# Kernel optimization log

Hardware: AMD Instinct MI355X
Metric: run time of the kernel (lower is better)

Reference implementation:

```python
import jax, jax.numpy as jnp
import numpy as np

B, T, D = 2, 2048, 1024
H = 16
DH = D // H            # 64, per-head dim
C = 128                # d_kv_compress
ROPE_BASE = 10000.0


def _rope_cos_sin(t_len, d_head, dtype):
    # freqs: (T, d_head/2); emb = cat(freqs, freqs) -> (T, d_head)
    inv_freq = 1.0 / (ROPE_BASE ** (jnp.arange(0, d_head, 2, dtype=jnp.float32) / d_head))
    freqs = jnp.arange(t_len, dtype=jnp.float32)[:, None] * inv_freq[None, :]
    emb = jnp.concatenate([freqs, freqs], axis=-1)
    return jnp.cos(emb).astype(dtype), jnp.sin(emb).astype(dtype)


def _rotate_half(x):
    x1, x2 = jnp.split(x, 2, axis=-1)
    return jnp.concatenate([-x2, x1], axis=-1)


def _apply_rope(x, cos, sin):
    # x: (B,H,T,DH); cos/sin: (T,DH)
    return x * cos[None, None] + _rotate_half(x) * sin[None, None]


def setup_inputs() -> dict:
    key = jax.random.key(0)
    ks = jax.random.split(key, 12)
    s = 0.02
    return {
        "x": jax.random.normal(ks[0], (B, T, D), dtype=jnp.float32),
        "w_dk": jax.random.normal(ks[1], (D, C), dtype=jnp.float32) * s,
        "b_dk": jnp.zeros((C,), dtype=jnp.float32),
        "w_dv": jax.random.normal(ks[2], (D, C), dtype=jnp.float32) * s,
        "b_dv": jnp.zeros((C,), dtype=jnp.float32),
        "w_uk": jax.random.normal(ks[3], (C, D), dtype=jnp.float32) * s,
        "b_uk": jnp.zeros((D,), dtype=jnp.float32),
        "w_uv": jax.random.normal(ks[4], (C, D), dtype=jnp.float32) * s,
        "b_uv": jnp.zeros((D,), dtype=jnp.float32),
        "w_o": jax.random.normal(ks[5], (D, D), dtype=jnp.float32) * s,
        "b_o": jnp.zeros((D,), dtype=jnp.float32),
    }


def reference(x, w_dk, b_dk, w_dv, b_dv, w_uk, b_uk, w_uv, b_uv, w_o, b_o):
    Bx, Tx, Dx = x.shape
    # low-rank KV compression then up-projection
    c_k = x @ w_dk + b_dk                      # (B,T,C)
    c_v = x @ w_dv + b_dv                      # (B,T,C)
    k = c_k @ w_uk + b_uk                      # (B,T,D)
    v = c_v @ w_uv + b_uv                      # (B,T,D)

    def split_heads(t):  # (B,T,D) -> (B,H,T,DH)
        return t.reshape(Bx, Tx, H, DH).transpose(0, 2, 1, 3)

    q = split_heads(x)
    k = split_heads(k)
    v = split_heads(v)

    cos, sin = _rope_cos_sin(Tx, DH, x.dtype)
    q = _apply_rope(q, cos, sin)
    k = _apply_rope(k, cos, sin)

    scale = 1.0 / np.sqrt(DH)
    attn = jnp.einsum('bhid,bhjd->bhij', q, k) * scale
    attn = jax.nn.softmax(attn, axis=-1)
    out = jnp.einsum('bhij,bhjd->bhid', attn, v)   # (B,H,T,DH)
    out = out.transpose(0, 2, 1, 3).reshape(Bx, Tx, Dx)
    return out @ w_o + b_o
```

## Files before the change

### kernel.cpp

```cpp
#include <hip/hip_runtime.h>
#include <hip/hip_bf16.h>
#include <math.h>

constexpr int kB  = 2;
constexpr int kT  = 2048;
constexpr int kD  = 1024;
constexpr int kH  = 16;
constexpr int kDH = 64;
constexpr int kC  = 128;
constexpr int kM  = kB * kT;
constexpr int kBH = kB * kH;

#define LOG10000_OVER_32 0.28782313662425575f
#define QSCALE 0.1803368801111773f

typedef unsigned short ushort_t;
using short8 = __attribute__((ext_vector_type(8))) short;
using f32x4  = __attribute__((ext_vector_type(4))) float;

__device__ inline ushort_t f2bf(float f) {
    __hip_bfloat16 h = __float2bfloat16(f);
    return *reinterpret_cast<ushort_t*>(&h);
}

__device__ inline short8 cvt8(const float* p) {
    float4 f0 = *reinterpret_cast<const float4*>(p);
    float4 f1 = *reinterpret_cast<const float4*>(p + 4);
    short8 v;
    v[0] = (short)f2bf(f0.x); v[1] = (short)f2bf(f0.y);
    v[2] = (short)f2bf(f0.z); v[3] = (short)f2bf(f0.w);
    v[4] = (short)f2bf(f1.x); v[5] = (short)f2bf(f1.y);
    v[6] = (short)f2bf(f1.z); v[7] = (short)f2bf(f1.w);
    return v;
}

__global__ __launch_bounds__(256)
void wtrans(const float* __restrict__ w_dk, const float* __restrict__ w_dv,
            const float* __restrict__ w_uk, const float* __restrict__ w_uv,
            const float* __restrict__ w_o,
            ushort_t* __restrict__ dkT, ushort_t* __restrict__ dvT,
            ushort_t* __restrict__ ukT, ushort_t* __restrict__ uvT,
            ushort_t* __restrict__ oT, float2* __restrict__ tab) {
    if (blockIdx.z == 5) {
        int flat = blockIdx.y * 32 + blockIdx.x;
        if (flat >= kT / 8) return;
        int t = flat * 8 + (threadIdx.x >> 5);
        int i = threadIdx.x & 31;
        float inv_freq = expf(-(float)i * LOG10000_OVER_32);
        float s, c;
        sincosf((float)t * inv_freq, &s, &c);
        tab[t * 32 + i] = make_float2(c, s);
        return;
    }
    const float* src; ushort_t* dst; int R, C;
    switch (blockIdx.z) {
        case 0: src = w_dk; dst = dkT; R = kD; C = kC; break;
        case 1: src = w_dv; dst = dvT; R = kD; C = kC; break;
        case 2: src = w_uk; dst = ukT; R = kC; C = kD; break;
        case 3: src = w_uv; dst = uvT; R = kC; C = kD; break;
        default: src = w_o; dst = oT;  R = kD; C = kD; break;
    }
    int c0 = blockIdx.x * 32, r0 = blockIdx.y * 32;
    if (c0 >= C || r0 >= R) return;

    __shared__ float Tl[32][33];
    int tx = threadIdx.x & 31, ty = threadIdx.x >> 5;
#pragma unroll
    for (int i = 0; i < 4; ++i)
        Tl[ty + 8 * i][tx] = src[(size_t)(r0 + ty + 8 * i) * C + c0 + tx];
    __syncthreads();
#pragma unroll
    for (int i = 0; i < 4; ++i)
        dst[(size_t)(c0 + ty + 8 * i) * R + r0 + tx] = f2bf(Tl[tx][ty + 8 * i]);
}

template<int MODE0, int MODE1>
__global__ __launch_bounds__(256)
void gemm_mfma(const ushort_t* __restrict__ A0_, const ushort_t* __restrict__ A1_,
               const ushort_t* __restrict__ Wt0, const float* __restrict__ bias0, void* __restrict__ C0,
               const ushort_t* __restrict__ Wt1, const float* __restrict__ bias1, void* __restrict__ C1,
               const float2* __restrict__ tab, int M, int N, int K) {
    constexpr int LDT = 40;
    __shared__ __align__(16) ushort_t As[128 * LDT];
    __shared__ __align__(16) ushort_t Bs[128 * LDT];

    const ushort_t* A    = blockIdx.z ? A1_ : A0_;
    const ushort_t* Wt   = blockIdx.z ? Wt1 : Wt0;
    const float*    bias = blockIdx.z ? bias1 : bias0;
    void*           Cc   = blockIdx.z ? C1 : C0;
    const int       mode = blockIdx.z ? MODE1 : MODE0;

    const int tid  = threadIdx.x;
    const int wave = tid >> 6, lane = tid & 63;
    const int g = lane >> 4, cl = lane & 15;
    const int m0 = blockIdx.y * 128, n0 = blockIdx.x * 128;
    const int wm = (wave >> 1) * 64, wn = (wave & 1) * 64;

    const int ar = tid >> 1;
    const int ac = (tid & 1) * 16;

    f32x4 acc[4][4] = {};

    for (int k0 = 0; k0 < K; k0 += 32) {
        {
            const ushort_t* Ab = A + (size_t)(m0 + ar) * K + k0 + ac;
            *reinterpret_cast<short8*>(&As[ar * LDT + ac])     = *reinterpret_cast<const short8*>(Ab);
            *reinterpret_cast<short8*>(&As[ar * LDT + ac + 8]) = *reinterpret_cast<const short8*>(Ab + 8);
            const ushort_t* Wb = Wt + (size_t)(n0 + ar) * K + k0 + ac;
            *reinterpret_cast<short8*>(&Bs[ar * LDT + ac])     = *reinterpret_cast<const short8*>(Wb);
            *reinterpret_cast<short8*>(&Bs[ar * LDT + ac + 8]) = *reinterpret_cast<const short8*>(Wb + 8);
        }
        __syncthreads();

        short8 a[4], b[4];
#pragma unroll
        for (int mi = 0; mi < 4; ++mi)
            a[mi] = *reinterpret_cast<const short8*>(&As[(wm + mi * 16 + cl) * LDT + g * 8]);
#pragma unroll
        for (int ni = 0; ni < 4; ++ni)
            b[ni] = *reinterpret_cast<const short8*>(&Bs[(wn + ni * 16 + cl) * LDT + g * 8]);
#pragma unroll
        for (int mi = 0; mi < 4; ++mi)
#pragma unroll
            for (int ni = 0; ni < 4; ++ni)
                acc[mi][ni] = __builtin_amdgcn_mfma_f32_16x16x32_bf16(a[mi], b[ni], acc[mi][ni], 0, 0, 0);
        __syncthreads();
    }

#pragma unroll
    for (int mi = 0; mi < 4; ++mi) {
        if (mode == 4) {
            const int h = (n0 + wn) >> 6;
#pragma unroll
            for (int r = 0; r < 4; ++r) {
                const int m = m0 + wm + mi * 16 + 4 * g + r;
                const int bb = m >> 11, t = m & (kT - 1);
                ushort_t* kp = (ushort_t*)Cc + (((size_t)bb * kH + h) * kT + t) * kDH;
#pragma unroll
                for (int pr = 0; pr < 2; ++pr) {
                    const int i = pr * 16 + cl;
                    float2 cs = tab[t * 32 + i];
                    float v1 = acc[mi][pr][r]     + bias[n0 + wn + pr * 16 + cl];
                    float v2 = acc[mi][pr + 2][r] + bias[n0 + wn + (pr + 2) * 16 + cl];
                    kp[i]      = f2bf(v1 * cs.x - v2 * cs.y);
                    kp[i + 32] = f2bf(v2 * cs.x + v1 * cs.y);
                }
            }
        } else {
#pragma unroll
            for (int ni = 0; ni < 4; ++ni) {
                const int mb = m0 + wm + mi * 16 + 4 * g;
                const int nn = n0 + wn + ni * 16 + cl;
                const float bv = bias[nn];
                const int h = nn >> 6, d = nn & (kDH - 1);
                const int bb = mb >> 11, t0 = mb & (kT - 1);
                uint2 u;
                u.x = (unsigned int)f2bf(acc[mi][ni][0] + bv) | ((unsigned int)f2bf(acc[mi][ni][1] + bv) << 16);
                u.y = (unsigned int)f2bf(acc[mi][ni][2] + bv) | ((unsigned int)f2bf(acc[mi][ni][3] + bv) << 16);
                ushort_t* vt = (ushort_t*)Cc;
                *reinterpret_cast<uint2*>(&vt[(((size_t)bb * kH + h) * kDH + d) * kT + t0]) = u;
            }
        }
    }
}

template<bool AF32, int MODE>
__global__ __launch_bounds__(256)
void gemm64(const void* __restrict__ A0_, const void* __restrict__ A1_,
            const ushort_t* __restrict__ Wt0, const float* __restrict__ bias0, void* __restrict__ C0,
            const ushort_t* __restrict__ Wt1, const float* __restrict__ bias1, void* __restrict__ C1,
            int M, int N, int K) {
    constexpr int LDT = 40;
    __shared__ __align__(16) ushort_t As[128 * LDT];
    __shared__ __align__(16) ushort_t Bs[64 * LDT];

    const void*     A    = blockIdx.z ? A1_ : A0_;
    const ushort_t* Wt   = blockIdx.z ? Wt1 : Wt0;
    const float*    bias = blockIdx.z ? bias1 : bias0;
    void*           Cc   = blockIdx.z ? C1 : C0;

    const int tid  = threadIdx.x;
    const int wave = tid >> 6, lane = tid & 63;
    const int g = lane >> 4, cl = lane & 15;
    const int m0 = blockIdx.y * 128, n0 = blockIdx.x * 64;
    const int wm = (wave >> 1) * 64, wn = (wave & 1) * 32;

    const int ar = tid >> 1, ac = (tid & 1) * 16;
    const int br = tid >> 2, bc = (tid & 3) * 8;

    f32x4 acc[4][2] = {};

    for (int k0 = 0; k0 < K; k0 += 32) {
        if constexpr (AF32) {
            const float* Af = (const float*)A + (size_t)(m0 + ar) * K + k0 + ac;
            *reinterpret_cast<short8*>(&As[ar * LDT + ac])     = cvt8(Af);
            *reinterpret_cast<short8*>(&As[ar * LDT + ac + 8]) = cvt8(Af + 8);
        } else {
            const ushort_t* Ab = (const ushort_t*)A + (size_t)(m0 + ar) * K + k0 + ac;
            *reinterpret_cast<short8*>(&As[ar * LDT + ac])     = *reinterpret_cast<const short8*>(Ab);
            *reinterpret_cast<short8*>(&As[ar * LDT + ac + 8]) = *reinterpret_cast<const short8*>(Ab + 8);
        }
        *reinterpret_cast<short8*>(&Bs[br * LDT + bc]) =
            *reinterpret_cast<const short8*>(Wt + (size_t)(n0 + br) * K + k0 + bc);
        __syncthreads();

        short8 a[4], b[2];
#pragma unroll
        for (int mi = 0; mi < 4; ++mi)
            a[mi] = *reinterpret_cast<const short8*>(&As[(wm + mi * 16 + cl) * LDT + g * 8]);
#pragma unroll
        for (int ni = 0; ni < 2; ++ni)
            b[ni] = *reinterpret_cast<const short8*>(&Bs[(wn + ni * 16 + cl) * LDT + g * 8]);
#pragma unroll
        for (int mi = 0; mi < 4; ++mi)
#pragma unroll
            for (int ni = 0; ni < 2; ++ni)
                acc[mi][ni] = __builtin_amdgcn_mfma_f32_16x16x32_bf16(a[mi], b[ni], acc[mi][ni], 0, 0, 0);
        __syncthreads();
    }

#pragma unroll
    for (int mi = 0; mi < 4; ++mi)
#pragma unroll
        for (int ni = 0; ni < 2; ++ni) {
            const int mb = m0 + wm + mi * 16 + 4 * g;
            const int nn = n0 + wn + ni * 16 + cl;
            const float bv = bias[nn];
            if constexpr (MODE == 0) {
#pragma unroll
                for (int r = 0; r < 4; ++r)
                    ((float*)Cc)[(size_t)(mb + r) * N + nn] = acc[mi][ni][r] + bv;
            } else {
#pragma unroll
                for (int r = 0; r < 4; ++r)
                    ((ushort_t*)Cc)[(size_t)(mb + r) * N + nn] = f2bf(acc[mi][ni][r] + bv);
            }
        }
}

__global__ __launch_bounds__(256)
void rope_split_q(const float* __restrict__ x, const float2* __restrict__ tab,
                  ushort_t* __restrict__ q_bf) {
    int idx = blockIdx.x * 256 + threadIdx.x;
    int i = idx & 31;
    int h = (idx >> 5) & (kH - 1);
    int t = (idx >> 9) & (kT - 1);
    int b = idx >> 20;

    const float* xp = x + ((size_t)(b * kT + t)) * kD + h * kDH;
    float x1 = xp[i];
    float x2 = xp[i + 32];
    float2 cs = tab[t * 32 + i];

    ushort_t* qp = q_bf + (((size_t)(b * kH + h)) * kT + t) * kDH;
    qp[i]      = f2bf((x1 * cs.x - x2 * cs.y) * QSCALE);
    qp[i + 32] = f2bf((x2 * cs.x + x1 * cs.y) * QSCALE);
}

__global__ __launch_bounds__(256)
void attn_mfma(const ushort_t* __restrict__ q_bf, const ushort_t* __restrict__ k_bf,
               const ushort_t* __restrict__ vt_bf,
               float* __restrict__ pacc, float* __restrict__ pl) {
    constexpr int LDV = 40;
    constexpr int LDP = 36;
    const int blk  = blockIdx.x;
    const int bh   = (blk & 7) * 4 + ((blk >> 3) & 3);
    const int half = (blk >> 5) & 1;
    const int qt   = blk >> 6;
    const int tid  = threadIdx.x;
    const int wave = tid >> 6, lane = tid & 63;
    const int g = lane >> 4, c = lane & 15;
    const int qbase = qt * 64 + wave * 16;

    __shared__ __align__(16) ushort_t Ks[32 * 64];
    __shared__ __align__(16) ushort_t Vs[64 * LDV];
    __shared__ __align__(16) ushort_t P_lds[4][16 * LDP];
    ushort_t* P = P_lds[wave];

    const ushort_t* qp = q_bf + ((size_t)bh * kT + qbase) * kDH;
    short8 qa0 = *reinterpret_cast<const short8*>(qp + (size_t)c * kDH + g * 8);
    short8 qa1 = *reinterpret_cast<const short8*>(qp + (size_t)c * kDH + g * 8 + 32);

    const ushort_t* kb = k_bf + (size_t)bh * kT * kDH;
    const ushort_t* vb = vt_bf + (size_t)bh * kDH * kT;

    const int kr_ = tid >> 3, kc_ = (tid & 7) * 8;
    const int ksw = kr_ * 64 + (kc_ ^ ((kr_ & 7) << 3));
    const int vr_ = tid >> 2, vc_ = (tid & 3) * 8;

    f32x4 acc[4] = {};
    float lsum[4] = {};

    const int kt0 = half * (kT / 2);
    for (int kt = kt0; kt < kt0 + kT / 2; kt += 32) {
        *reinterpret_cast<short8*>(&Ks[ksw]) =
            *reinterpret_cast<const short8*>(&kb[(size_t)(kt + kr_) * kDH + kc_]);
        *reinterpret_cast<short8*>(&Vs[vr_ * LDV + vc_]) =
            *reinterpret_cast<const short8*>(&vb[(size_t)vr_ * kT + kt + vc_]);
        __syncthreads();

        short8 kf[2][2];
#pragma unroll
        for (int kj = 0; kj < 2; ++kj)
#pragma unroll
            for (int f = 0; f < 2; ++f) {
                const int row = kj * 16 + c;
                const int col = f * 32 + g * 8;
                kf[kj][f] = *reinterpret_cast<const short8*>(
                    &Ks[row * 64 + (col ^ ((row & 7) << 3))]);
            }

        f32x4 z = {0.f, 0.f, 0.f, 0.f};
        f32x4 s0 = __builtin_amdgcn_mfma_f32_16x16x32_bf16(qa0, kf[0][0], z, 0, 0, 0);
        s0 = __builtin_amdgcn_mfma_f32_16x16x32_bf16(qa1, kf[0][1], s0, 0, 0, 0);
        f32x4 s1 = __builtin_amdgcn_mfma_f32_16x16x32_bf16(qa0, kf[1][0], z, 0, 0, 0);
        s1 = __builtin_amdgcn_mfma_f32_16x16x32_bf16(qa1, kf[1][1], s1, 0, 0, 0);

#pragma unroll
        for (int r = 0; r < 4; ++r) {
            float p0 = exp2f(s0[r]);
            float p1 = exp2f(s1[r]);
            lsum[r] += p0 + p1;
            P[(4 * g + r) * LDP + c]      = f2bf(p0);
            P[(4 * g + r) * LDP + 16 + c] = f2bf(p1);
        }
        short8 pa = *reinterpret_cast<const short8*>(&P[c * LDP + g * 8]);

        short8 vf[4];
#pragma unroll
        for (int n = 0; n < 4; ++n)
            vf[n] = *reinterpret_cast<const short8*>(&Vs[(16 * n + c) * LDV + g * 8]);
#pragma unroll
        for (int n = 0; n < 4; ++n)
            acc[n] = __builtin_amdgcn_mfma_f32_16x16x32_bf16(pa, vf[n], acc[n], 0, 0, 0);
        __syncthreads();
    }

#pragma unroll
    for (int off = 1; off < 16; off <<= 1)
#pragma unroll
        for (int r = 0; r < 4; ++r)
            lsum[r] += __shfl_xor(lsum[r], off, 64);

#pragma unroll
    for (int r = 0; r < 4; ++r) {
        size_t row = ((size_t)(half * kBH + bh) * kT + qbase + 4 * g + r) * kDH;
#pragma unroll
        for (int n = 0; n < 4; ++n)
            pacc[row + 16 * n + c] = acc[n][r];
    }
    if (c == 0) {
#pragma unroll
        for (int r = 0; r < 4; ++r)
            pl[(size_t)(half * kBH + bh) * kT + qbase + 4 * g + r] = lsum[r];
    }
}

__global__ __launch_bounds__(256)
void attn_combine(const float* __restrict__ pacc, const float* __restrict__ pl,
                  ushort_t* __restrict__ att_bf) {
    int flat = blockIdx.x * 256 + threadIdx.x;
    int d4 = (flat & 15) * 4;
    int t  = (flat >> 4) & (kT - 1);
    int bh = flat >> 15;
    int b = bh >> 4, h = bh & (kH - 1);

    size_t i0 = ((size_t)bh * kT + t) * kDH + d4;
    size_t i1 = ((size_t)(kBH + bh) * kT + t) * kDH + d4;
    float4 a0 = *reinterpret_cast<const float4*>(&pacc[i0]);
    float4 a1 = *reinterpret_cast<const float4*>(&pacc[i1]);
    float inv = 1.0f / (pl[(size_t)bh * kT + t] + pl[(size_t)(kBH + bh) * kT + t]);

    uint2 u;
    u.x = (unsigned int)f2bf((a0.x + a1.x) * inv) | ((unsigned int)f2bf((a0.y + a1.y) * inv) << 16);
    u.y = (unsigned int)f2bf((a0.z + a1.z) * inv) | ((unsigned int)f2bf((a0.w + a1.w) * inv) << 16);
    ushort_t* op = att_bf + ((size_t)(b * kT + t)) * kD + h * kDH + d4;
    *reinterpret_cast<uint2*>(op) = u;
}

extern "C" void kernel_launch(void* const* d_in, const int* in_sizes, int n_in,
                              void* d_out, int out_size, void* d_ws, size_t ws_size,
                              hipStream_t stream) {
    const float* x    = (const float*)d_in[0];
    const float* w_dk = (const float*)d_in[1];
    const float* b_dk = (const float*)d_in[2];
    const float* w_dv = (const float*)d_in[3];
    const float* b_dv = (const float*)d_in[4];
    const float* w_uk = (const float*)d_in[5];
    const float* b_uk = (const float*)d_in[6];
    const float* w_uv = (const float*)d_in[7];
    const float* b_uv = (const float*)d_in[8];
    const float* w_o  = (const float*)d_in[9];
    const float* b_o  = (const float*)d_in[10];
    float* out = (float*)d_out;

    char* w = (char*)d_ws;
    ushort_t* q_bf   = (ushort_t*)w;  w += (size_t)kM * kD * 2;
    ushort_t* k_bf   = (ushort_t*)w;  w += (size_t)kM * kD * 2;
    ushort_t* vt_bf  = (ushort_t*)w;  w += (size_t)kM * kD * 2;
    ushort_t* ckbf   = (ushort_t*)w;  w += (size_t)kM * kC * 2;
    ushort_t* cvbf   = (ushort_t*)w;  w += (size_t)kM * kC * 2;
    ushort_t* dkT    = (ushort_t*)w;  w += (size_t)kC * kD * 2;
    ushort_t* dvT    = (ushort_t*)w;  w += (size_t)kC * kD * 2;
    ushort_t* ukT    = (ushort_t*)w;  w += (size_t)kD * kC * 2;
    ushort_t* uvT    = (ushort_t*)w;  w += (size_t)kD * kC * 2;
    ushort_t* oT     = (ushort_t*)w;  w += (size_t)kD * kD * 2;
    float2*   tab    = (float2*)w;    w += (size_t)kT * 32 * 8;
    float*    pacc   = (float*)w;     w += (size_t)2 * kBH * kT * kDH * 4;
    float*    pl     = (float*)w;     w += (size_t)2 * kBH * kT * 4;

    dim3 blk(256);

    wtrans<<<dim3(32, 32, 6), blk, 0, stream>>>(w_dk, w_dv, w_uk, w_uv, w_o,
                                                dkT, dvT, ukT, uvT, oT, tab);

    gemm64<true, 3><<<dim3(kC / 64, kM / 128, 2), blk, 0, stream>>>(
        x, x, dkT, b_dk, ckbf, dvT, b_dv, cvbf, kM, kC, kD);

    gemm_mfma<4, 2><<<dim3(kD / 128, kM / 128, 2), blk, 0, stream>>>(
        ckbf, cvbf, ukT, b_uk, k_bf, uvT, b_uv, vt_bf, tab, kM, kD, kC);

    rope_split_q<<<(kB * kT * kH * 32) / 256, blk, 0, stream>>>(x, tab, q_bf);

    attn_mfma<<<dim3(kT / 64 * kBH * 2), blk, 0, stream>>>(q_bf, k_bf, vt_bf, pacc, pl);

    attn_combine<<<dim3(kBH * kT * kDH / (4 * 256)), blk, 0, stream>>>(pacc, pl, q_bf);

    gemm64<false, 0><<<dim3(kD / 64, kM / 128, 1), blk, 0, stream>>>(
        q_bf, q_bf, oT, b_o, out, oT, b_o, out, kM, kD, kD);
}
```

Baseline: 256.2 us.

## Drop split-KV attention; normalize in-kernel and remove combine pass

Each attention block now walks the full key sequence instead of half of it. The softmax normalization and bf16 output write move into the attention kernel, which removes the fp32 partial-accumulator buffers and the separate combine kernel. The K tile switches from an XOR swizzle to a padded row stride, and P uses an unpadded layout. The cost is half as many blocks (1024 vs 2048) with twice the serial loop length, which lowers parallelism. The unpadded P layout may also bring LDS bank conflicts.

Measured after the change: 235.6 us. -8.0%, faster.

```diff
diff --git a/kernel.cpp b/kernel.cpp
--- a/kernel.cpp
+++ b/kernel.cpp
@@ -259,23 +259,22 @@
 
 __global__ __launch_bounds__(256)
 void attn_mfma(const ushort_t* __restrict__ q_bf, const ushort_t* __restrict__ k_bf,
-               const ushort_t* __restrict__ vt_bf,
-               float* __restrict__ pacc, float* __restrict__ pl) {
+               const ushort_t* __restrict__ vt_bf, ushort_t* __restrict__ att_bf) {
+    constexpr int LDK = 72;
     constexpr int LDV = 40;
-    constexpr int LDP = 36;
     const int blk  = blockIdx.x;
     const int bh   = (blk & 7) * 4 + ((blk >> 3) & 3);
-    const int half = (blk >> 5) & 1;
-    const int qt   = blk >> 6;
+    const int qt   = blk >> 5;
     const int tid  = threadIdx.x;
-    const int wave = tid >> 6, lane = tid & 63;
+    const int wave = tid >> 6;
+    const int lane = tid & 63;
     const int g = lane >> 4, c = lane & 15;
     const int qbase = qt * 64 + wave * 16;
 
-    __shared__ __align__(16) ushort_t Ks[32 * 64];
+    __shared__ __align__(16) ushort_t Ks[32 * LDK];
     __shared__ __align__(16) ushort_t Vs[64 * LDV];
-    __shared__ __align__(16) ushort_t P_lds[4][16 * LDP];
-    ushort_t* P = P_lds[wave];
+    __shared__ __align__(16) ushort_t P_lds[4][16][32];
+    ushort_t (*P)[32] = P_lds[wave];
 
     const ushort_t* qp = q_bf + ((size_t)bh * kT + qbase) * kDH;
     short8 qa0 = *reinterpret_cast<const short8*>(qp + (size_t)c * kDH + g * 8);
@@ -285,46 +284,43 @@
     const ushort_t* vb = vt_bf + (size_t)bh * kDH * kT;
 
     const int kr_ = tid >> 3, kc_ = (tid & 7) * 8;
-    const int ksw = kr_ * 64 + (kc_ ^ ((kr_ & 7) << 3));
     const int vr_ = tid >> 2, vc_ = (tid & 3) * 8;
 
     f32x4 acc[4] = {};
-    float lsum[4] = {};
-
-    const int kt0 = half * (kT / 2);
-    for (int kt = kt0; kt < kt0 + kT / 2; kt += 32) {
-        *reinterpret_cast<short8*>(&Ks[ksw]) =
+    float lsum[4] = {0.f, 0.f, 0.f, 0.f};
+
+    for (int kt = 0; kt < kT; kt += 32) {
+        *reinterpret_cast<short8*>(&Ks[kr_ * LDK + kc_]) =
             *reinterpret_cast<const short8*>(&kb[(size_t)(kt + kr_) * kDH + kc_]);
         *reinterpret_cast<short8*>(&Vs[vr_ * LDV + vc_]) =
             *reinterpret_cast<const short8*>(&vb[(size_t)vr_ * kT + kt + vc_]);
         __syncthreads();
 
-        short8 kf[2][2];
-#pragma unroll
-        for (int kj = 0; kj < 2; ++kj)
-#pragma unroll
-            for (int f = 0; f < 2; ++f) {
-                const int row = kj * 16 + c;
-                const int col = f * 32 + g * 8;
-                kf[kj][f] = *reinterpret_cast<const short8*>(
-                    &Ks[row * 64 + (col ^ ((row & 7) << 3))]);
-            }
+        short8 k00 = *reinterpret_cast<const short8*>(&Ks[c * LDK + g * 8]);
+        short8 k01 = *reinterpret_cast<const short8*>(&Ks[c * LDK + 32 + g * 8]);
+        short8 k10 = *reinterpret_cast<const short8*>(&Ks[(16 + c) * LDK + g * 8]);
+        short8 k11 = *reinterpret_cast<const short8*>(&Ks[(16 + c) * LDK + 32 + g * 8]);
 
         f32x4 z = {0.f, 0.f, 0.f, 0.f};
-        f32x4 s0 = __builtin_amdgcn_mfma_f32_16x16x32_bf16(qa0, kf[0][0], z, 0, 0, 0);
-        s0 = __builtin_amdgcn_mfma_f32_16x16x32_bf16(qa1, kf[0][1], s0, 0, 0, 0);
-        f32x4 s1 = __builtin_amdgcn_mfma_f32_16x16x32_bf16(qa0, kf[1][0], z, 0, 0, 0);
-        s1 = __builtin_amdgcn_mfma_f32_16x16x32_bf16(qa1, kf[1][1], s1, 0, 0, 0);
-
+        f32x4 s0 = __builtin_amdgcn_mfma_f32_16x16x32_bf16(qa0, k00, z, 0, 0, 0);
+        s0 = __builtin_amdgcn_mfma_f32_16x16x32_bf16(qa1, k01, s0, 0, 0, 0);
+        f32x4 s1 = __builtin_amdgcn_mfma_f32_16x16x32_bf16(qa0, k10, z, 0, 0, 0);
+        s1 = __builtin_amdgcn_mfma_f32_16x16x32_bf16(qa1, k11, s1, 0, 0, 0);
+
+        float p0[4], p1[4];
 #pragma unroll
         for (int r = 0; r < 4; ++r) {
-            float p0 = exp2f(s0[r]);
-            float p1 = exp2f(s1[r]);
-            lsum[r] += p0 + p1;
-            P[(4 * g + r) * LDP + c]      = f2bf(p0);
-            P[(4 * g + r) * LDP + 16 + c] = f2bf(p1);
-        }
-        short8 pa = *reinterpret_cast<const short8*>(&P[c * LDP + g * 8]);
+            p0[r] = exp2f(s0[r]);
+            p1[r] = exp2f(s1[r]);
+            lsum[r] += p0[r] + p1[r];
+        }
+
+#pragma unroll
+        for (int r = 0; r < 4; ++r) {
+            P[4 * g + r][c]      = f2bf(p0[r]);
+            P[4 * g + r][16 + c] = f2bf(p1[r]);
+        }
+        short8 pa = *reinterpret_cast<const short8*>(&P[c][g * 8]);
 
         short8 vf[4];
 #pragma unroll
@@ -339,43 +335,17 @@
 #pragma unroll
     for (int off = 1; off < 16; off <<= 1)
 #pragma unroll
-        for (int r = 0; r < 4; ++r)
-            lsum[r] += __shfl_xor(lsum[r], off, 64);
-
+        for (int r = 0; r < 4; ++r) lsum[r] += __shfl_xor(lsum[r], off, 64);
+
+    const int b = bh >> 4, h = bh & (kH - 1);
 #pragma unroll
     for (int r = 0; r < 4; ++r) {
-        size_t row = ((size_t)(half * kBH + bh) * kT + qbase + 4 * g + r) * kDH;
+        float inv_l = 1.0f / lsum[r];
+        size_t row = (size_t)(b * kT + qbase + 4 * g + r) * kD + h * kDH;
 #pragma unroll
         for (int n = 0; n < 4; ++n)
-            pacc[row + 16 * n + c] = acc[n][r];
-    }
-    if (c == 0) {
-#pragma unroll
-        for (int r = 0; r < 4; ++r)
-            pl[(size_t)(half * kBH + bh) * kT + qbase + 4 * g + r] = lsum[r];
-    }
-}
-
-__global__ __launch_bounds__(256)
-void attn_combine(const float* __restrict__ pacc, const float* __restrict__ pl,
-                  ushort_t* __restrict__ att_bf) {
-    int flat = blockIdx.x * 256 + threadIdx.x;
-    int d4 = (flat & 15) * 4;
-    int t  = (flat >> 4) & (kT - 1);
-    int bh = flat >> 15;
-    int b = bh >> 4, h = bh & (kH - 1);
-
-    size_t i0 = ((size_t)bh * kT + t) * kDH + d4;
-    size_t i1 = ((size_t)(kBH + bh) * kT + t) * kDH + d4;
-    float4 a0 = *reinterpret_cast<const float4*>(&pacc[i0]);
-    float4 a1 = *reinterpret_cast<const float4*>(&pacc[i1]);
-    float inv = 1.0f / (pl[(size_t)bh * kT + t] + pl[(size_t)(kBH + bh) * kT + t]);
-
-    uint2 u;
-    u.x = (unsigned int)f2bf((a0.x + a1.x) * inv) | ((unsigned int)f2bf((a0.y + a1.y) * inv) << 16);
-    u.y = (unsigned int)f2bf((a0.z + a1.z) * inv) | ((unsigned int)f2bf((a0.w + a1.w) * inv) << 16);
-    ushort_t* op = att_bf + ((size_t)(b * kT + t)) * kD + h * kDH + d4;
-    *reinterpret_cast<uint2*>(op) = u;
+            att_bf[row + 16 * n + c] = f2bf(acc[n][r] * inv_l);
+    }
 }
 
 extern "C" void kernel_launch(void* const* d_in, const int* in_sizes, int n_in,
@@ -398,6 +368,7 @@
     ushort_t* q_bf   = (ushort_t*)w;  w += (size_t)kM * kD * 2;
     ushort_t* k_bf   = (ushort_t*)w;  w += (size_t)kM * kD * 2;
     ushort_t* vt_bf  = (ushort_t*)w;  w += (size_t)kM * kD * 2;
+    ushort_t* att_bf = (ushort_t*)w;  w += (size_t)kM * kD * 2;
     ushort_t* ckbf   = (ushort_t*)w;  w += (size_t)kM * kC * 2;
     ushort_t* cvbf   = (ushort_t*)w;  w += (size_t)kM * kC * 2;
     ushort_t* dkT    = (ushort_t*)w;  w += (size_t)kC * kD * 2;
@@ -406,8 +377,6 @@
     ushort_t* uvT    = (ushort_t*)w;  w += (size_t)kD * kC * 2;
     ushort_t* oT     = (ushort_t*)w;  w += (size_t)kD * kD * 2;
     float2*   tab    = (float2*)w;    w += (size_t)kT * 32 * 8;
-    float*    pacc   = (float*)w;     w += (size_t)2 * kBH * kT * kDH * 4;
-    float*    pl     = (float*)w;     w += (size_t)2 * kBH * kT * 4;
 
     dim3 blk(256);
 
@@ -422,10 +391,8 @@
 
     rope_split_q<<<(kB * kT * kH * 32) / 256, blk, 0, stream>>>(x, tab, q_bf);
 
-    attn_mfma<<<dim3(kT / 64 * kBH * 2), blk, 0, stream>>>(q_bf, k_bf, vt_bf, pacc, pl);
-
-    attn_combine<<<dim3(kBH * kT * kDH / (4 * 256)), blk, 0, stream>>>(pacc, pl, q_bf);
+    attn_mfma<<<dim3(kT / 64 * kBH), blk, 0, stream>>>(q_bf, k_bf, vt_bf, att_bf);
 
     gemm64<false, 0><<<dim3(kD / 64, kM / 128, 1), blk, 0, stream>>>(
-        q_bf, q_bf, oT, b_o, out, oT, b_o, out, kM, kD, kD);
-}
+        att_bf, att_bf, oT, b_o, out, oT, b_o, out, kM, kD, kD);
+}
```
